# Optimization experiments

Hardware: AMD Instinct MI355X
Metric: run time of the kernel (lower is better)

Reference implementation:

```python
import math
import jax, jax.numpy as jnp
import numpy as np

SCALES = (128.0, 256.0, 512.0)
ASPECT_RATIOS = (0.5, 1.0, 2.0)
NMS_THR = 0.7
PRENMS_K = 6000   # rpn_test_prenms_topk (module built with training=False)
POST_K = 300      # rpn_test_topk
MIN_SIZE = 16.0
DW_CLIP = math.log(1000.0 / 16.0)


def conv2d(x, w, b, pad):
    y = jax.lax.conv_general_dilated(
        x, w, window_strides=(1, 1), padding=[(pad, pad), (pad, pad)],
        dimension_numbers=("NCHW", "OIHW", "NCHW"))
    return y + b[None, :, None, None]


def generate_anchors(im_h, im_w, grid_h, grid_w, dtype):
    stride_h = float(im_h // grid_h)
    stride_w = float(im_w // grid_w)
    ar = jnp.asarray(ASPECT_RATIOS, dtype)
    sc = jnp.asarray(SCALES, dtype)
    h_ratios = jnp.sqrt(ar)
    w_ratios = 1.0 / h_ratios
    hs = (h_ratios[:, None] * sc[None, :]).reshape(-1)   # [A]
    ws = (w_ratios[:, None] * sc[None, :]).reshape(-1)
    base = jnp.round(jnp.stack([-ws, -hs, ws, hs], axis=1) / 2.0)  # [A,4]
    xs = jnp.arange(grid_w, dtype=dtype) * stride_w
    ys = jnp.arange(grid_h, dtype=dtype) * stride_h
    sy, sx = jnp.meshgrid(ys, xs, indexing="ij")
    sx = sx.reshape(-1); sy = sy.reshape(-1)
    shift = jnp.stack([sx, sy, sx, sy], axis=1)           # [HW,4]
    return (shift[:, None, :] + base[None, :, :]).reshape(-1, 4)  # [HW*A,4]


def decode_boxes(pred, anchors):
    # pred, anchors: [N,4] -> decoded [N,4]
    w = anchors[:, 2] - anchors[:, 0]
    h = anchors[:, 3] - anchors[:, 1]
    cx = anchors[:, 0] + 0.5 * w
    cy = anchors[:, 1] + 0.5 * h
    dx, dy = pred[:, 0], pred[:, 1]
    dw = jnp.minimum(pred[:, 2], DW_CLIP)
    dh = jnp.minimum(pred[:, 3], DW_CLIP)
    px = dx * w + cx
    py = dy * h + cy
    pw = jnp.exp(dw) * w
    ph = jnp.exp(dh) * h
    return jnp.stack([px - 0.5 * pw, py - 0.5 * ph, px + 0.5 * pw, py + 0.5 * ph], axis=1)


def nms_keep(boxes, valid, thr):
    # boxes assumed sorted by descending score; sequential greedy NMS.
    N = boxes.shape[0]
    area = (boxes[:, 2] - boxes[:, 0]) * (boxes[:, 3] - boxes[:, 1])
    idx = jnp.arange(N)

    def body(i, keep):
        b = jax.lax.dynamic_slice(boxes, (i, 0), (1, 4))[0]
        x1 = jnp.maximum(b[0], boxes[:, 0])
        y1 = jnp.maximum(b[1], boxes[:, 1])
        x2 = jnp.minimum(b[2], boxes[:, 2])
        y2 = jnp.minimum(b[3], boxes[:, 3])
        inter = jnp.clip(x2 - x1, 0.0) * jnp.clip(y2 - y1, 0.0)
        iou = inter / (area[i] + area - inter)
        suppress = (iou > thr) & (idx > i) & keep[i]
        return keep & ~suppress

    return jax.lax.fori_loop(0, N, body, valid)


def rpn_forward(image, feat, rpn_conv_w, rpn_conv_b, cls_w, cls_b, bbox_w, bbox_b):
    rpn_feat = jax.nn.relu(conv2d(feat, rpn_conv_w, rpn_conv_b, pad=1))
    cls_scores = conv2d(rpn_feat, cls_w, cls_b, pad=0)       # [B,A,H,W]
    box_pred = conv2d(rpn_feat, bbox_w, bbox_b, pad=0)       # [B,4A,H,W]
    B, A, H, W = cls_scores.shape
    im_h, im_w = image.shape[-2], image.shape[-1]
    anchors = generate_anchors(im_h, im_w, H, W, feat.dtype)  # [HWA,4]

    cls_flat = jnp.transpose(cls_scores, (0, 2, 3, 1)).reshape(-1)              # [B*H*W*A]
    pred = jnp.transpose(box_pred.reshape(B, A, 4, H, W), (0, 3, 4, 1, 2)).reshape(-1, 4)
    proposals = decode_boxes(pred, anchors)                   # [N,4]

    scores = jax.nn.sigmoid(cls_flat)
    top_scores, top_idx = jax.lax.top_k(scores, PRENMS_K)
    props = proposals[top_idx]                                # [K,4]
    # clamp to image boundary
    props = jnp.stack([
        jnp.clip(props[:, 0], 0.0, float(im_w)),
        jnp.clip(props[:, 1], 0.0, float(im_h)),
        jnp.clip(props[:, 2], 0.0, float(im_w)),
        jnp.clip(props[:, 3], 0.0, float(im_h))], axis=1)
    w = props[:, 2] - props[:, 0]
    h = props[:, 3] - props[:, 1]
    valid = (w >= MIN_SIZE) & (h >= MIN_SIZE)
    keep = nms_keep(props, valid, NMS_THR)                    # already score-sorted
    masked = jnp.where(keep, top_scores, -jnp.inf)
    final_scores, sel = jax.lax.top_k(masked, POST_K)
    final_boxes = props[sel]
    ok = jnp.isfinite(final_scores)
    final_boxes = jnp.where(ok[:, None], final_boxes, 0.0)
    final_scores = jnp.where(ok, final_scores, 0.0)
    return jnp.concatenate([final_boxes, final_scores[:, None]], axis=1)  # [POST_K,5]


def setup_inputs() -> dict:
    key = jax.random.key(0)
    ks = jax.random.split(key, 6)
    C, H, W, A = 256, 128, 128, 9
    IMH = IMW = 1024
    std = 0.01
    return {
        "image": jax.random.normal(ks[0], (1, 3, IMH, IMW), jnp.float32),
        "feat": jax.random.normal(ks[1], (1, C, H, W), jnp.float32),
        "rpn_conv_w": jax.random.normal(ks[2], (C, C, 3, 3), jnp.float32) * std,
        "rpn_conv_b": jnp.zeros((C,), jnp.float32),
        "cls_w": jax.random.normal(ks[3], (A, C, 1, 1), jnp.float32) * std,
        "cls_b": jnp.zeros((A,), jnp.float32),
        "bbox_w": jax.random.normal(ks[4], (4 * A, C, 1, 1), jnp.float32) * std,
        "bbox_b": jnp.zeros((4 * A,), jnp.float32),
    }


def reference(image, feat, rpn_conv_w, rpn_conv_b, cls_w, cls_b, bbox_w, bbox_b):
    return rpn_forward(image, feat, rpn_conv_w, rpn_conv_b, cls_w, cls_b, bbox_w, bbox_b)
```

## Files before the change

kernel.cpp:

```cpp
#include <hip/hip_runtime.h>

#define HW 128
#define NPIX 16384
#define CIN 256
#define NSC 147456
#define PRENMS 6000
#define POSTK 300
#define DW_CLIP_F 4.135166556742356f
#define MW 96
typedef unsigned long long ull;

__global__ void prep_kernel(const float* __restrict__ w, float* __restrict__ wt,
                            const float* __restrict__ cls_w, const float* __restrict__ bbox_w,
                            float* __restrict__ wh45,
                            unsigned* __restrict__ zp, int nz) {
    int i = blockIdx.x * 256 + threadIdx.x;
    if (i < nz) zp[i] = 0u;
    if (i < 11520) {
        int ci = i / 45, s = i - ci * 45;
        wh45[i] = (s < 9) ? cls_w[s * CIN + ci] : bbox_w[(s - 9) * CIN + ci];
    }
    if (i < 2304 * 256) {
        int k = i >> 8, co = i & 255;
        wt[i] = w[co * 2304 + k];
    }
}

__global__ __launch_bounds__(64, 8) void conv3x3_kernel(
    const float* __restrict__ feat, const float* __restrict__ wt,
    float* __restrict__ part)
{
    __shared__ float in_s[8 * 114];
    const int l = threadIdx.x;
    const int sp = blockIdx.x;
    const int x0 = (sp & 7) * 16;
    const int y0 = (sp >> 3) * 4;
    const int co0 = blockIdx.y * 16;
    const int h = blockIdx.z;
    const int tx = l & 15, ty = l >> 4;

    const int r1 = l / 18, c1 = l - r1 * 18;
    const int e2 = l + 64;
    const int r2 = e2 / 18, c2 = e2 - r2 * 18;
    const int gy1 = y0 + r1 - 1, gx1 = x0 + c1 - 1;
    const int gy2 = y0 + r2 - 1, gx2 = x0 + c2 - 1;
    const bool q1 = ((unsigned)gy1 < 128u) && ((unsigned)gx1 < 128u);
    const bool q2 = (l < 44) && ((unsigned)gy2 < 128u) && ((unsigned)gx2 < 128u);
    const int a1 = q1 ? (gy1 * 128 + gx1) : 0;
    const int a2 = q2 ? (gy2 * 128 + gx2) : 0;
    const int d1 = r1 * 19 + c1;
    const int d2 = r2 * 19 + c2;

    float acc[16];
#pragma unroll
    for (int i = 0; i < 16; ++i) acc[i] = 0.f;

    const float* fh = feat + h * 128 * NPIX;
    const float* whp = wt + h * 128 * 9 * 256 + co0;

    for (int s = 0; s < 16; ++s) {
        const float* fb = fh + s * 8 * NPIX;
#pragma unroll
        for (int ci = 0; ci < 8; ++ci) {
            float f1 = fb[ci * NPIX + a1];
            in_s[ci * 114 + d1] = q1 ? f1 : 0.f;
            if (l < 44) {
                float f2 = fb[ci * NPIX + a2];
                in_s[ci * 114 + d2] = q2 ? f2 : 0.f;
            }
        }
        const float* ws0 = whp + s * 8 * 9 * 256;
#pragma unroll
        for (int ci = 0; ci < 8; ++ci) {
#pragma unroll
            for (int t = 0; t < 9; ++t) {
                const int ky = t / 3, kx = t - ky * 3;
                float v = in_s[ci * 114 + (ty + ky) * 19 + (tx + kx)];
                const float* wp = ws0 + (ci * 9 + t) * 256;
#pragma unroll
                for (int co = 0; co < 16; ++co)
                    acc[co] = fmaf(v, wp[co], acc[co]);
            }
        }
    }
    float* po = part + h * (CIN * NPIX) + co0 * NPIX + (y0 + ty) * 128 + x0 + tx;
#pragma unroll
    for (int co = 0; co < 16; ++co)
        po[co * NPIX] = acc[co];
}

__global__ __launch_bounds__(256) void heads_kernel(
    const float* __restrict__ part, const float* __restrict__ conv_b,
    const float* __restrict__ wh45,
    const float* __restrict__ cls_b, const float* __restrict__ bbox_b,
    float* __restrict__ scores, float* __restrict__ bb)
{
    __shared__ float partial[3][64][46];
    const int t = threadIdx.x;
    const int lane = t & 63, q = t >> 6;
    const int p = blockIdx.x * 64 + lane;
    const float* p0 = part + p;
    const float* p1 = part + CIN * NPIX + p;
    const int cb = q * 64;

    float acc[45];
#pragma unroll
    for (int i = 0; i < 45; ++i) acc[i] = 0.f;

    float va[4], vb[4];
#pragma unroll
    for (int k = 0; k < 4; ++k) {
        va[k] = p0[(cb + k) * NPIX];
        vb[k] = p1[(cb + k) * NPIX];
    }
#pragma unroll 4
    for (int i = 0; i < 64; ++i) {
        const int ci = cb + i;
        float v = fmaxf(va[i & 3] + vb[i & 3] + conv_b[ci], 0.f);
        if (i + 4 < 64) {
            va[i & 3] = p0[(ci + 4) * NPIX];
            vb[i & 3] = p1[(ci + 4) * NPIX];
        }
        const float* wr = wh45 + ci * 45;
#pragma unroll
        for (int s = 0; s < 45; ++s)
            acc[s] = fmaf(v, wr[s], acc[s]);
    }
    if (q) {
#pragma unroll
        for (int s = 0; s < 45; ++s) partial[q - 1][lane][s] = acc[s];
    }
    __syncthreads();
    if (q == 0) {
#pragma unroll
        for (int s = 0; s < 45; ++s) {
            float r = acc[s] + partial[0][lane][s];
            r += partial[1][lane][s];
            r += partial[2][lane][s];
            acc[s] = r;
        }
#pragma unroll
        for (int a = 0; a < 9; ++a) {
            float s = acc[a] + cls_b[a];
            scores[p * 9 + a] = 1.0f / (1.0f + expf(-s));
        }
#pragma unroll
        for (int c = 0; c < 36; ++c) {
            bb[c * NPIX + p] = acc[9 + c] + bbox_b[c];
        }
    }
}

__global__ __launch_bounds__(1024) void hist1_kernel(const float* __restrict__ scores,
                                                     unsigned* __restrict__ hist1) {
    __shared__ unsigned h[16384];
    const int tid = threadIdx.x;
    for (int i = tid; i < 16384; i += 1024) h[i] = 0u;
    __syncthreads();
    for (int i = blockIdx.x * 1024 + tid; i < NSC; i += gridDim.x * 1024) {
        unsigned bits = __float_as_uint(scores[i]);
        atomicAdd(&h[bits >> 16], 1u);
    }
    __syncthreads();
    for (int i = tid; i < 16384; i += 1024) {
        unsigned c = h[i];
        if (c) atomicAdd(&hist1[i], c);
    }
}

__global__ __launch_bounds__(1024) void scan1_kernel(const unsigned* __restrict__ hist,
                                                     unsigned* __restrict__ meta) {
    __shared__ unsigned ssum[1024];
    const int t = threadIdx.x;
    unsigned local[16];
    unsigned s = 0;
#pragma unroll
    for (int i = 0; i < 16; ++i) { local[i] = hist[t * 16 + i]; s += local[i]; }
    ssum[t] = s;
    __syncthreads();
    for (int off = 1; off < 1024; off <<= 1) {
        unsigned v = ssum[t] + ((t + off < 1024) ? ssum[t + off] : 0u);
        __syncthreads();
        ssum[t] = v;
        __syncthreads();
    }
    unsigned run = ssum[t] - s;
#pragma unroll
    for (int i = 15; i >= 0; --i) {
        unsigned nb = run + local[i];
        if (nb >= (unsigned)PRENMS && run < (unsigned)PRENMS) {
            meta[1] = (unsigned)(t * 16 + i);
            meta[2] = run;
        }
        run = nb;
    }
}

__global__ void hist2_kernel(const float* __restrict__ scores, const unsigned* __restrict__ meta,
                             unsigned* __restrict__ hist2) {
    int i = blockIdx.x * 256 + threadIdx.x;
    if (i < NSC) {
        unsigned bits = __float_as_uint(scores[i]);
        if ((bits >> 16) == meta[1]) atomicAdd(&hist2[bits & 0xFFFFu], 1u);
    }
}

__global__ __launch_bounds__(1024) void scan2_kernel(const unsigned* __restrict__ hist2,
                                                     unsigned* __restrict__ meta) {
    __shared__ unsigned ssum[1024];
    const int t = threadIdx.x;
    const unsigned need = (unsigned)PRENMS - meta[2];
    unsigned s = 0;
    for (int i = 0; i < 64; ++i) s += hist2[t * 64 + i];
    ssum[t] = s;
    __syncthreads();
    for (int off = 1; off < 1024; off <<= 1) {
        unsigned v = ssum[t] + ((t + off < 1024) ? ssum[t + off] : 0u);
        __syncthreads();
        ssum[t] = v;
        __syncthreads();
    }
    unsigned run = ssum[t] - s;
    for (int i = 63; i >= 0; --i) {
        unsigned h = hist2[t * 64 + i];
        unsigned nb = run + h;
        if (nb >= need && run < need) {
            meta[3] = (meta[1] << 16) | (unsigned)(t * 64 + i);
        }
        run = nb;
    }
}

__global__ void compact_kernel(const float* __restrict__ scores, unsigned* __restrict__ meta,
                               ull* __restrict__ cand) {
    int i = blockIdx.x * 256 + threadIdx.x;
    unsigned bits = (i < NSC) ? __float_as_uint(scores[i]) : 0u;
    bool pred = (i < NSC) && (bits >= meta[3]);
    ull bal = __ballot(pred);
    int lane = threadIdx.x & 63;
    unsigned cnt = (unsigned)__popcll(bal);
    unsigned base = 0;
    if (lane == 0 && cnt) base = atomicAdd(&meta[0], cnt);
    base = __shfl(base, 0);
    if (pred) {
        unsigned off = (unsigned)__popcll(bal & ((1ull << lane) - 1ull));
        unsigned pos = base + off;
        if (pos < 8192u)
            cand[pos] = ((ull)bits << 32) | (unsigned)(~i);
    }
}

__global__ __launch_bounds__(1024) void sortA_kernel(const ull* __restrict__ cand,
                                                     const unsigned* __restrict__ meta,
                                                     ull* __restrict__ sorted) {
    __shared__ ull keys[2048];
    const int tid = threadIdx.x;
    const int base = blockIdx.x * 2048;
    const int n = min((int)meta[0], 8192);
    for (int i = tid; i < 2048; i += 1024) {
        int g = base + i;
        keys[i] = (g < n) ? cand[g] : (ull)(8191 - g);
    }
    __syncthreads();
    for (int k = 2; k <= 2048; k <<= 1) {
        for (int j = k >> 1; j >= 1; j >>= 1) {
            int s = tid;
            int i = ((s & ~(j - 1)) << 1) | (s & (j - 1));
            int p = i | j;
            ull a = keys[i], c = keys[p];
            bool desc = ((i & k) == 0);
            bool sw = desc ? (a < c) : (a > c);
            if (sw) { keys[i] = c; keys[p] = a; }
            __syncthreads();
        }
    }
    for (int i = tid; i < 2048; i += 1024) sorted[base + i] = keys[i];
}

__global__ __launch_bounds__(256) void merge_decode_kernel(
    const ull* __restrict__ sorted, const float* __restrict__ bb,
    float* __restrict__ selbox, float* __restrict__ selsc,
    ull* __restrict__ validbits)
{
    const int g = blockIdx.x * 256 + threadIdx.x;
    ull key = sorted[g];
    const int c = g >> 11;
    int rank = g & 2047;
#pragma unroll
    for (int cc = 0; cc < 4; ++cc) {
        if (cc == c) continue;
        const ull* arr = sorted + cc * 2048;
        int lo = 0, hi = 2048;
        while (lo < hi) { int mid = (lo + hi) >> 1; if (arr[mid] > key) lo = mid + 1; else hi = mid; }
        rank += lo;
    }
    if (rank >= PRENMS) return;
    unsigned sbits = (unsigned)(key >> 32);
    unsigned idx = ~(unsigned)(key & 0xFFFFFFFFull);
    float score = __uint_as_float(sbits);
    int p = (int)(idx / 9u);
    int a = (int)(idx - (unsigned)p * 9u);
    int y = p >> 7, x = p & 127;
    float d0 = bb[(a * 4 + 0) * NPIX + p];
    float d1 = bb[(a * 4 + 1) * NPIX + p];
    float d2 = bb[(a * 4 + 2) * NPIX + p];
    float d3 = bb[(a * 4 + 3) * NPIX + p];
    int ar_i = a / 3, sc_i = a - ar_i * 3;
    float arv = (ar_i == 0) ? 0.5f : ((ar_i == 1) ? 1.0f : 2.0f);
    float scv = (sc_i == 0) ? 128.f : ((sc_i == 1) ? 256.f : 512.f);
    float hr = sqrtf(arv);
    float wr = 1.0f / hr;
    float hs = hr * scv;
    float wsv = wr * scv;
    float bx1 = rintf(-wsv * 0.5f), by1 = rintf(-hs * 0.5f);
    float bx2 = rintf(wsv * 0.5f),  by2 = rintf(hs * 0.5f);
    float ax1 = x * 8.f + bx1, ay1 = y * 8.f + by1;
    float ax2 = x * 8.f + bx2, ay2 = y * 8.f + by2;
    float wa = ax2 - ax1, ha = ay2 - ay1;
    float cx = ax1 + 0.5f * wa, cy = ay1 + 0.5f * ha;
    float dw = fminf(d2, DW_CLIP_F), dh = fminf(d3, DW_CLIP_F);
    float px = d0 * wa + cx, py = d1 * ha + cy;
    float pw = expf(dw) * wa, ph = expf(dh) * ha;
    float x1 = px - 0.5f * pw, y1 = py - 0.5f * ph;
    float x2 = px + 0.5f * pw, y2 = py + 0.5f * ph;
    x1 = fminf(fmaxf(x1, 0.f), 1024.f);
    y1 = fminf(fmaxf(y1, 0.f), 1024.f);
    x2 = fminf(fmaxf(x2, 0.f), 1024.f);
    y2 = fminf(fmaxf(y2, 0.f), 1024.f);
    float bw = x2 - x1, bh = y2 - y1;
    selbox[rank * 4 + 0] = x1; selbox[rank * 4 + 1] = y1;
    selbox[rank * 4 + 2] = x2; selbox[rank * 4 + 3] = y2;
    selsc[rank] = score;
    if ((bw >= 16.f) && (bh >= 16.f))
        atomicOr(&validbits[rank >> 6], 1ull << (rank & 63));
}

__global__ __launch_bounds__(256) void maskbuild_kernel(
    const float* __restrict__ selbox, ull* __restrict__ mask)
{
    __shared__ float jb0[64], jb1[64], jb2[64], jb3[64];
    const int jw = blockIdx.y;
    const int tid = threadIdx.x;
    const int i = blockIdx.x * 256 + tid;
    if (jw * 64 + 63 < blockIdx.x * 256) {
        if (i < PRENMS) mask[(size_t)i * MW + jw] = 0ull;
        return;
    }
    if (tid < 64) {
        int j = jw * 64 + tid;
        float x1 = 0.f, y1 = 0.f, x2 = 0.f, y2 = 0.f;
        if (j < PRENMS) {
            x1 = selbox[j * 4 + 0]; y1 = selbox[j * 4 + 1];
            x2 = selbox[j * 4 + 2]; y2 = selbox[j * 4 + 3];
        }
        jb0[tid] = x1; jb1[tid] = y1; jb2[tid] = x2; jb3[tid] = y2;
    }
    __syncthreads();
    if (i >= PRENMS) return;
    const float ix1 = selbox[i * 4 + 0], iy1 = selbox[i * 4 + 1];
    const float ix2 = selbox[i * 4 + 2], iy2 = selbox[i * 4 + 3];
    const float iarea = (ix2 - ix1) * (iy2 - iy1);
    ull word = 0ull;
    for (int b = 0; b < 64; ++b) {
        int j = jw * 64 + b;
        float xx1 = fmaxf(ix1, jb0[b]);
        float yy1 = fmaxf(iy1, jb1[b]);
        float xx2 = fminf(ix2, jb2[b]);
        float yy2 = fminf(iy2, jb3[b]);
        float iw = fmaxf(xx2 - xx1, 0.f);
        float ih = fmaxf(yy2 - yy1, 0.f);
        float inter = iw * ih;
        float jarea = (jb2[b] - jb0[b]) * (jb3[b] - jb1[b]);
        float iou = inter / (iarea + jarea - inter);
        if (j > i && iou > 0.7f) word |= (1ull << b);
    }
    mask[(size_t)i * MW + jw] = word;
}

__global__ __launch_bounds__(64) void nms_scan_kernel(
    const ull* __restrict__ validbits,
    const ull* __restrict__ mask,
    const float* __restrict__ selbox, const float* __restrict__ selsc,
    float* __restrict__ out)
{
    __shared__ int kept[POSTK];
    const int l = threadIdx.x;
    ull supp0 = ~validbits[l];
    ull supp1 = (l < 30) ? ~validbits[64 + l] : ~0ull;
    int nk = 0;
    ull ownrow_next = mask[(size_t)l * MW + 0];
    for (int wi = 0; wi < 94 && nk < POSTK; ++wi) {
        ull ownrow = ownrow_next;
        if (wi < 93) ownrow_next = mask[(size_t)((wi + 1) * 64 + l) * MW + (wi + 1)];
        ull wsup = (wi < 64) ? __shfl(supp0, wi) : __shfl(supp1, wi - 64);
        ull active = ~wsup;
        if (!active) continue;
        ull keptbits = 0ull;
        while (active && nk < POSTK) {
            int b = __builtin_ctzll(active);
            keptbits |= (1ull << b);
            if (l == 0) kept[nk] = wi * 64 + b;
            nk++;
            ull rowb = __shfl(ownrow, b);
            ull gt = (b == 63) ? 0ull : (~0ull << (b + 1));
            active &= gt & ~rowb;
        }
        while (keptbits) {
            int b0 = __builtin_ctzll(keptbits); keptbits &= keptbits - 1;
            int b1 = -1, b2 = -1, b3 = -1;
            if (keptbits) { b1 = __builtin_ctzll(keptbits); keptbits &= keptbits - 1; }
            if (keptbits) { b2 = __builtin_ctzll(keptbits); keptbits &= keptbits - 1; }
            if (keptbits) { b3 = __builtin_ctzll(keptbits); keptbits &= keptbits - 1; }
            const ull* r0 = mask + (size_t)(wi * 64 + b0) * MW;
            ull t0a = r0[l], t0b = (l < 30) ? r0[64 + l] : 0ull;
            ull t1a = 0, t1b = 0, t2a = 0, t2b = 0, t3a = 0, t3b = 0;
            if (b1 >= 0) { const ull* r1 = mask + (size_t)(wi * 64 + b1) * MW; t1a = r1[l]; t1b = (l < 30) ? r1[64 + l] : 0ull; }
            if (b2 >= 0) { const ull* r2 = mask + (size_t)(wi * 64 + b2) * MW; t2a = r2[l]; t2b = (l < 30) ? r2[64 + l] : 0ull; }
            if (b3 >= 0) { const ull* r3 = mask + (size_t)(wi * 64 + b3) * MW; t3a = r3[l]; t3b = (l < 30) ? r3[64 + l] : 0ull; }
            supp0 |= t0a | t1a | t2a | t3a;
            supp1 |= t0b | t1b | t2b | t3b;
        }
    }
    __syncthreads();
    for (int r = l; r < POSTK; r += 64) {
        if (r < nk) {
            int i = kept[r];
            out[r * 5 + 0] = selbox[i * 4 + 0];
            out[r * 5 + 1] = selbox[i * 4 + 1];
            out[r * 5 + 2] = selbox[i * 4 + 2];
            out[r * 5 + 3] = selbox[i * 4 + 3];
            out[r * 5 + 4] = selsc[i];
        } else {
            out[r * 5 + 0] = 0.f; out[r * 5 + 1] = 0.f;
            out[r * 5 + 2] = 0.f; out[r * 5 + 3] = 0.f;
            out[r * 5 + 4] = 0.f;
        }
    }
}

extern "C" void kernel_launch(void* const* d_in, const int* in_sizes, int n_in,
                              void* d_out, int out_size, void* d_ws, size_t ws_size,
                              hipStream_t stream) {
    const float* feat    = (const float*)d_in[1];
    const float* conv_w  = (const float*)d_in[2];
    const float* conv_b  = (const float*)d_in[3];
    const float* cls_w   = (const float*)d_in[4];
    const float* cls_b   = (const float*)d_in[5];
    const float* bbox_w  = (const float*)d_in[6];
    const float* bbox_b  = (const float*)d_in[7];
    float* out = (float*)d_out;

    char* ws = (char*)d_ws;
    float*    part      = (float*)(ws + 0);
    float*    wt        = (float*)(ws + 33554432);
    float*    wh45      = (float*)(ws + 35913728);
    float*    bb        = (float*)(ws + 35959808);
    float*    scores    = (float*)(ws + 38319104);
    unsigned* hist1     = (unsigned*)(ws + 38908928);
    unsigned* hist2     = (unsigned*)(ws + 38974464);
    unsigned* meta      = (unsigned*)(ws + 39236608);
    ull*      validbits = (ull*)(ws + 39236864);
    ull*      cand      = (ull*)(ws + 39237632);
    ull*      sorted    = (ull*)(ws + 39303168);
    float*    selbox    = (float*)(ws + 39368704);
    float*    selsc     = (float*)(ws + 39464960);
    ull*      mask      = (ull*)(ws + 39489024);

    const int nz = 16384 + 65536 + 64 + 192;
    prep_kernel<<<2304, 256, 0, stream>>>(conv_w, wt, cls_w, bbox_w, wh45, hist1, nz);
    conv3x3_kernel<<<dim3(256, 16, 2), 64, 0, stream>>>(feat, wt, part);
    heads_kernel<<<256, 256, 0, stream>>>(part, conv_b, wh45, cls_b, bbox_b, scores, bb);
    hist1_kernel<<<64, 1024, 0, stream>>>(scores, hist1);
    scan1_kernel<<<1, 1024, 0, stream>>>(hist1, meta);
    hist2_kernel<<<(NSC + 255) / 256, 256, 0, stream>>>(scores, meta, hist2);
    scan2_kernel<<<1, 1024, 0, stream>>>(hist2, meta);
    compact_kernel<<<(NSC + 255) / 256, 256, 0, stream>>>(scores, meta, cand);
    sortA_kernel<<<4, 1024, 0, stream>>>(cand, meta, sorted);
    merge_decode_kernel<<<32, 256, 0, stream>>>(sorted, bb, selbox, selsc, validbits);
    maskbuild_kernel<<<dim3(24, 94), 256, 0, stream>>>(selbox, mask);
    nms_scan_kernel<<<1, 64, 0, stream>>>(validbits, mask, selbox, selsc, out);
}
```

Baseline: 597.3 us.

## Restructure conv3x3 into 16x16 tiles without LDS, fuse histogram scans into last-block

The 3x3 conv now uses 256-thread blocks covering 16x16 pixel tiles. Each thread loads its nine input taps straight from global memory instead of staging a halo in shared memory, and boundary tiles take a separate masked path. The two scan kernels are folded into the histogram kernels using a last-block-done atomic counter, which removes two launches. This trades shared-memory reuse for cache-reliant global loads, and hist2 now runs 64 grid-stride blocks. The new counters meta[4] and meta[5] must be zero at start; they appear to sit inside the zeroed prep range.

Result: slower. 623.2 us (+4.3%).

```diff
diff --git a/kernel.cpp b/kernel.cpp
--- a/kernel.cpp
+++ b/kernel.cpp
@@ -26,64 +26,71 @@
     }
 }
 
-__global__ __launch_bounds__(64, 8) void conv3x3_kernel(
+__global__ __launch_bounds__(256) void conv3x3_kernel(
     const float* __restrict__ feat, const float* __restrict__ wt,
     float* __restrict__ part)
 {
-    __shared__ float in_s[8 * 114];
-    const int l = threadIdx.x;
-    const int sp = blockIdx.x;
-    const int x0 = (sp & 7) * 16;
-    const int y0 = (sp >> 3) * 4;
-    const int co0 = blockIdx.y * 16;
-    const int h = blockIdx.z;
-    const int tx = l & 15, ty = l >> 4;
-
-    const int r1 = l / 18, c1 = l - r1 * 18;
-    const int e2 = l + 64;
-    const int r2 = e2 / 18, c2 = e2 - r2 * 18;
-    const int gy1 = y0 + r1 - 1, gx1 = x0 + c1 - 1;
-    const int gy2 = y0 + r2 - 1, gx2 = x0 + c2 - 1;
-    const bool q1 = ((unsigned)gy1 < 128u) && ((unsigned)gx1 < 128u);
-    const bool q2 = (l < 44) && ((unsigned)gy2 < 128u) && ((unsigned)gx2 < 128u);
-    const int a1 = q1 ? (gy1 * 128 + gx1) : 0;
-    const int a2 = q2 ? (gy2 * 128 + gx2) : 0;
-    const int d1 = r1 * 19 + c1;
-    const int d2 = r2 * 19 + c2;
+    const int tx = threadIdx.x, ty = threadIdx.y;
+    const int x0 = blockIdx.x * 16, y0 = blockIdx.y * 16;
+    const int h = blockIdx.z >> 4;
+    const int co0 = (blockIdx.z & 15) << 4;
+    const int px = x0 + tx, py = y0 + ty;
 
     float acc[16];
 #pragma unroll
     for (int i = 0; i < 16; ++i) acc[i] = 0.f;
 
     const float* fh = feat + h * 128 * NPIX;
-    const float* whp = wt + h * 128 * 9 * 256 + co0;
-
-    for (int s = 0; s < 16; ++s) {
-        const float* fb = fh + s * 8 * NPIX;
-#pragma unroll
-        for (int ci = 0; ci < 8; ++ci) {
-            float f1 = fb[ci * NPIX + a1];
-            in_s[ci * 114 + d1] = q1 ? f1 : 0.f;
-            if (l < 44) {
-                float f2 = fb[ci * NPIX + a2];
-                in_s[ci * 114 + d2] = q2 ? f2 : 0.f;
-            }
-        }
-        const float* ws0 = whp + s * 8 * 9 * 256;
-#pragma unroll
-        for (int ci = 0; ci < 8; ++ci) {
+    const float* wh = wt + h * 128 * 9 * 256 + co0;
+
+    const bool interior = (x0 > 0) && (y0 > 0) && (x0 < 112) && (y0 < 112);
+
+    if (interior) {
+        const float* fb = fh + (py - 1) * 128 + (px - 1);
+#pragma unroll 2
+        for (int ci = 0; ci < 128; ++ci) {
+            const float* f = fb + ci * NPIX;
+            float v[9];
 #pragma unroll
             for (int t = 0; t < 9; ++t) {
                 const int ky = t / 3, kx = t - ky * 3;
-                float v = in_s[ci * 114 + (ty + ky) * 19 + (tx + kx)];
-                const float* wp = ws0 + (ci * 9 + t) * 256;
+                v[t] = f[ky * 128 + kx];
+            }
+            const float* wp = wh + ci * 9 * 256;
+#pragma unroll
+            for (int t = 0; t < 9; ++t) {
 #pragma unroll
                 for (int co = 0; co < 16; ++co)
-                    acc[co] = fmaf(v, wp[co], acc[co]);
+                    acc[co] = fmaf(v[t], wp[t * 256 + co], acc[co]);
             }
         }
-    }
-    float* po = part + h * (CIN * NPIX) + co0 * NPIX + (y0 + ty) * 128 + x0 + tx;
+    } else {
+        int off[9];
+        float okf[9];
+#pragma unroll
+        for (int t = 0; t < 9; ++t) {
+            const int ky = t / 3 - 1, kx = t - (t / 3) * 3 - 1;
+            const int gy = py + ky, gx = px + kx;
+            const bool ok = ((unsigned)gy < 128u) && ((unsigned)gx < 128u);
+            off[t] = ok ? (gy * 128 + gx) : 0;
+            okf[t] = ok ? 1.f : 0.f;
+        }
+#pragma unroll 2
+        for (int ci = 0; ci < 128; ++ci) {
+            const float* f = fh + ci * NPIX;
+            float v[9];
+#pragma unroll
+            for (int t = 0; t < 9; ++t) v[t] = f[off[t]] * okf[t];
+            const float* wp = wh + ci * 9 * 256;
+#pragma unroll
+            for (int t = 0; t < 9; ++t) {
+#pragma unroll
+                for (int co = 0; co < 16; ++co)
+                    acc[co] = fmaf(v[t], wp[t * 256 + co], acc[co]);
+            }
+        }
+    }
+    float* po = part + h * (CIN * NPIX) + co0 * NPIX + py * 128 + px;
 #pragma unroll
     for (int co = 0; co < 16; ++co)
         po[co * NPIX] = acc[co];
@@ -152,80 +159,84 @@
 }
 
 __global__ __launch_bounds__(1024) void hist1_kernel(const float* __restrict__ scores,
-                                                     unsigned* __restrict__ hist1) {
+                                                     unsigned* __restrict__ hist1,
+                                                     unsigned* __restrict__ meta) {
     __shared__ unsigned h[16384];
+    __shared__ unsigned lastflag;
     const int tid = threadIdx.x;
     for (int i = tid; i < 16384; i += 1024) h[i] = 0u;
     __syncthreads();
-    for (int i = blockIdx.x * 1024 + tid; i < NSC; i += gridDim.x * 1024) {
-        unsigned bits = __float_as_uint(scores[i]);
-        atomicAdd(&h[bits >> 16], 1u);
+    for (int i = blockIdx.x * 1024 + tid; i < NSC; i += 64 * 1024) {
+        atomicAdd(&h[__float_as_uint(scores[i]) >> 16], 1u);
     }
     __syncthreads();
     for (int i = tid; i < 16384; i += 1024) {
         unsigned c = h[i];
         if (c) atomicAdd(&hist1[i], c);
     }
-}
-
-__global__ __launch_bounds__(1024) void scan1_kernel(const unsigned* __restrict__ hist,
-                                                     unsigned* __restrict__ meta) {
-    __shared__ unsigned ssum[1024];
-    const int t = threadIdx.x;
+    __threadfence();
+    if (tid == 0) lastflag = (atomicAdd(&meta[4], 1u) == 63u) ? 1u : 0u;
+    __syncthreads();
+    if (!lastflag) return;
+    const volatile unsigned* vh = (const volatile unsigned*)hist1;
     unsigned local[16];
     unsigned s = 0;
 #pragma unroll
-    for (int i = 0; i < 16; ++i) { local[i] = hist[t * 16 + i]; s += local[i]; }
-    ssum[t] = s;
+    for (int i = 0; i < 16; ++i) { local[i] = vh[tid * 16 + i]; s += local[i]; }
+    __syncthreads();
+    h[tid] = s;
     __syncthreads();
     for (int off = 1; off < 1024; off <<= 1) {
-        unsigned v = ssum[t] + ((t + off < 1024) ? ssum[t + off] : 0u);
+        unsigned v = h[tid] + ((tid + off < 1024) ? h[tid + off] : 0u);
         __syncthreads();
-        ssum[t] = v;
+        h[tid] = v;
         __syncthreads();
     }
-    unsigned run = ssum[t] - s;
+    unsigned run = h[tid] - s;
 #pragma unroll
     for (int i = 15; i >= 0; --i) {
         unsigned nb = run + local[i];
         if (nb >= (unsigned)PRENMS && run < (unsigned)PRENMS) {
-            meta[1] = (unsigned)(t * 16 + i);
+            meta[1] = (unsigned)(tid * 16 + i);
             meta[2] = run;
         }
         run = nb;
     }
 }
 
-__global__ void hist2_kernel(const float* __restrict__ scores, const unsigned* __restrict__ meta,
-                             unsigned* __restrict__ hist2) {
-    int i = blockIdx.x * 256 + threadIdx.x;
-    if (i < NSC) {
+__global__ __launch_bounds__(1024) void hist2_kernel(const float* __restrict__ scores,
+                                                     unsigned* __restrict__ meta,
+                                                     unsigned* __restrict__ hist2) {
+    __shared__ unsigned ss[1024];
+    __shared__ unsigned lastflag;
+    const int tid = threadIdx.x;
+    const unsigned b1 = meta[1];
+    for (int i = blockIdx.x * 1024 + tid; i < NSC; i += 64 * 1024) {
         unsigned bits = __float_as_uint(scores[i]);
-        if ((bits >> 16) == meta[1]) atomicAdd(&hist2[bits & 0xFFFFu], 1u);
-    }
-}
-
-__global__ __launch_bounds__(1024) void scan2_kernel(const unsigned* __restrict__ hist2,
-                                                     unsigned* __restrict__ meta) {
-    __shared__ unsigned ssum[1024];
-    const int t = threadIdx.x;
+        if ((bits >> 16) == b1) atomicAdd(&hist2[bits & 0xFFFFu], 1u);
+    }
+    __threadfence();
+    if (tid == 0) lastflag = (atomicAdd(&meta[5], 1u) == 63u) ? 1u : 0u;
+    __syncthreads();
+    if (!lastflag) return;
+    const volatile unsigned* vh = (const volatile unsigned*)hist2;
     const unsigned need = (unsigned)PRENMS - meta[2];
+    unsigned local[64];
     unsigned s = 0;
-    for (int i = 0; i < 64; ++i) s += hist2[t * 64 + i];
-    ssum[t] = s;
+    for (int i = 0; i < 64; ++i) { local[i] = vh[tid * 64 + i]; s += local[i]; }
+    ss[tid] = s;
     __syncthreads();
     for (int off = 1; off < 1024; off <<= 1) {
-        unsigned v = ssum[t] + ((t + off < 1024) ? ssum[t + off] : 0u);
+        unsigned v = ss[tid] + ((tid + off < 1024) ? ss[tid + off] : 0u);
         __syncthreads();
-        ssum[t] = v;
+        ss[tid] = v;
         __syncthreads();
     }
-    unsigned run = ssum[t] - s;
+    unsigned run = ss[tid] - s;
     for (int i = 63; i >= 0; --i) {
-        unsigned h = hist2[t * 64 + i];
-        unsigned nb = run + h;
+        unsigned nb = run + local[i];
         if (nb >= need && run < need) {
-            meta[3] = (meta[1] << 16) | (unsigned)(t * 64 + i);
+            meta[3] = (b1 << 16) | (unsigned)(tid * 64 + i);
         }
         run = nb;
     }
@@ -468,12 +479,10 @@
 
     const int nz = 16384 + 65536 + 64 + 192;
     prep_kernel<<<2304, 256, 0, stream>>>(conv_w, wt, cls_w, bbox_w, wh45, hist1, nz);
-    conv3x3_kernel<<<dim3(256, 16, 2), 64, 0, stream>>>(feat, wt, part);
+    conv3x3_kernel<<<dim3(8, 8, 32), dim3(16, 16), 0, stream>>>(feat, wt, part);
     heads_kernel<<<256, 256, 0, stream>>>(part, conv_b, wh45, cls_b, bbox_b, scores, bb);
-    hist1_kernel<<<64, 1024, 0, stream>>>(scores, hist1);
-    scan1_kernel<<<1, 1024, 0, stream>>>(hist1, meta);
-    hist2_kernel<<<(NSC + 255) / 256, 256, 0, stream>>>(scores, meta, hist2);
-    scan2_kernel<<<1, 1024, 0, stream>>>(hist2, meta);
+    hist1_kernel<<<64, 1024, 0, stream>>>(scores, hist1, meta);
+    hist2_kernel<<<64, 1024, 0, stream>>>(scores, meta, hist2);
     compact_kernel<<<(NSC + 255) / 256, 256, 0, stream>>>(scores, meta, cand);
     sortA_kernel<<<4, 1024, 0, stream>>>(cand, meta, sorted);
     merge_decode_kernel<<<32, 256, 0, stream>>>(sorted, bb, selbox, selsc, validbits);
```
